# Kernel tuning notes

Measured on AMD Instinct MI355X. Metric: run time of the kernel, lower is better.

Reference implementation:

```python
import jax, jax.numpy as jnp
import numpy as np

P = 2          # feature power
K = 128        # top-k neighbors
ALPHA = 1.0
BETA = 1.0
EPS = 1e-12


def _smooth_rank_l2(v):
    # v: [B, r]. torch: relu(-(v[:,None,:] - v[:,:,None])).sum(-1)
    # element [b,i,j] of diff = v[b,j] - v[b,i]; relu(-diff) = relu(v[b,i]-v[b,j])
    return jnp.sum(jax.nn.relu(v[:, :, None] - v[:, None, :]), axis=-1)  # [B, r]


def setup_inputs() -> dict:
    key = jax.random.key(0)
    k1, k2, k3 = jax.random.split(key, 3)
    B, d, N0 = 256, 2048, 7936
    return {
        "f_s": jax.random.normal(k1, (B, d), dtype=jnp.float32),
        "f_t": jax.random.normal(k2, (B, d), dtype=jnp.float32),
        "gallery": jax.random.normal(k3, (N0, d), dtype=jnp.float32),
    }


def reference(f_s, f_t, gallery):
    # pool='all': x.pow(p).view(B, -1)
    fs = f_s ** P                      # [B, d]
    ft = f_t ** P                      # [B, d]
    # statistics=True, layer 0: teacher_features = concat(existing, f_t)
    gal = jnp.concatenate([gallery, ft], axis=0)   # [N, d]

    d2 = (jnp.sum(ft * ft, axis=-1, keepdims=True)
          + jnp.sum(gal * gal, axis=-1)[None, :]
          - 2.0 * ft @ gal.T)                       # [B, N]
    tt_dist = jnp.sqrt(jnp.clip(d2, EPS, None))

    # k smallest distances (torch.sort ascending + slice [:k])
    neg_top, top_k_index = jax.lax.top_k(-tt_dist, K)
    t_value = -neg_top                               # [B, K], ascending

    # per-row re-gather of gallery and student-to-gallery distances
    gal_k = gal[top_k_index]                         # [B, K, d]
    s_d2 = (jnp.sum(fs * fs, axis=-1)[:, None]
            + jnp.sum(gal_k * gal_k, axis=-1)
            - 2.0 * jnp.einsum('bd,bkd->bk', fs, gal_k))
    s_value = jnp.sqrt(jnp.clip(s_d2, EPS, None))    # [B, K]

    main_loss = ALPHA * jnp.mean(jnp.abs(s_value[:, 0] - t_value[:, 0]))

    r = K - 1
    t_rank = _smooth_rank_l2(t_value[:, 1:])         # [B, r]
    s_rank = _smooth_rank_l2(s_value[:, 1:])         # [B, r]
    extra_loss = BETA * jnp.mean(jnp.linalg.norm(t_rank - s_rank, axis=1)) / r

    return main_loss + extra_loss
```

## Files before the change

### kernel.cpp

```cpp
#include <hip/hip_runtime.h>
#include <hip/hip_bf16.h>

#define BDIM 256
#define DDIM 2048
#define NGAL 7936
#define NTOT 8192
#define TOPK 128
#define EPSC 1e-12f

typedef __attribute__((ext_vector_type(8))) short bf16x8;
typedef __attribute__((ext_vector_type(4))) float f32x4;
typedef unsigned long long u64;

__device__ __forceinline__ short bfr(float x) {
  unsigned u = __float_as_uint(x);
  unsigned r = (u + 0x7FFFu + ((u >> 16) & 1u)) >> 16;
  return (short)r;
}

__global__ __launch_bounds__(256) void k_prep(
    const float* __restrict__ f_t, const float* __restrict__ f_s,
    short* __restrict__ Abf, short* __restrict__ Bbf,
    float* __restrict__ normA, float* __restrict__ galnorm) {
  int b = blockIdx.x, t = threadIdx.x;
  const float4* t4 = (const float4*)(f_t + (size_t)b * DDIM);
  const float4* s4 = (const float4*)(f_s + (size_t)b * DDIM);
  float st = 0.f, ss = 0.f;
  for (int i = t; i < DDIM / 4; i += 256) {
    float4 v = t4[i];
    float4 q = make_float4(v.x * v.x, v.y * v.y, v.z * v.z, v.w * v.w);
    short4 qb = make_short4(bfr(q.x), bfr(q.y), bfr(q.z), bfr(q.w));
    *(short4*)&Abf[(size_t)b * DDIM + i * 4] = qb;
    *(short4*)&Bbf[(size_t)(NGAL + b) * DDIM + i * 4] = qb;
    st += q.x * q.x + q.y * q.y + q.z * q.z + q.w * q.w;
    float4 u_ = s4[i];
    float4 r = make_float4(u_.x * u_.x, u_.y * u_.y, u_.z * u_.z, u_.w * u_.w);
    *(short4*)&Abf[(size_t)(BDIM + b) * DDIM + i * 4] =
        make_short4(bfr(r.x), bfr(r.y), bfr(r.z), bfr(r.w));
    ss += r.x * r.x + r.y * r.y + r.z * r.z + r.w * r.w;
  }
  for (int off = 32; off; off >>= 1) {
    st += __shfl_xor(st, off);
    ss += __shfl_xor(ss, off);
  }
  __shared__ float red[8];
  int lane = t & 63, wv = t >> 6;
  if (lane == 0) { red[wv] = st; red[4 + wv] = ss; }
  __syncthreads();
  if (t == 0) {
    float a = red[0] + red[1] + red[2] + red[3];
    float c = red[4] + red[5] + red[6] + red[7];
    normA[b] = a;
    galnorm[NGAL + b] = a;
    normA[BDIM + b] = c;
  }
}

__global__ __launch_bounds__(256) void k_galn(
    const float* __restrict__ gallery, short* __restrict__ Bbf,
    float* __restrict__ galnorm) {
  int row = blockIdx.x * 4 + (threadIdx.x >> 6);
  int lane = threadIdx.x & 63;
  const float4* g4 = (const float4*)(gallery + (size_t)row * DDIM);
  float s = 0.f;
  for (int i = lane; i < DDIM / 4; i += 64) {
    float4 v = g4[i];
    *(short4*)&Bbf[(size_t)row * DDIM + i * 4] =
        make_short4(bfr(v.x), bfr(v.y), bfr(v.z), bfr(v.w));
    s += v.x * v.x + v.y * v.y + v.z * v.z + v.w * v.w;
  }
  for (int off = 32; off; off >>= 1) s += __shfl_xor(s, off);
  if (lane == 0) galnorm[row] = s;
}

__global__ __launch_bounds__(256) void k_gemm(
    const short* __restrict__ Abf, const short* __restrict__ Bbf,
    const float* __restrict__ normA, const float* __restrict__ galnorm,
    float* __restrict__ d2) {
  __shared__ short As[2][128 * 64];
  __shared__ short Bs[2][128 * 64];
  int t = threadIdx.x;
  int n0 = blockIdx.x * 128, m0 = blockIdx.y * 128;
  int lane = t & 63, wid = t >> 6;
  int wm = wid >> 1, wn = wid & 1;

  const short* Ag = Abf + (size_t)m0 * DDIM;
  const short* Bg = Bbf + (size_t)n0 * DDIM;

  int j = t & 7, rb_ = t >> 3;
  size_t gofs = (size_t)rb_ * DDIM + j * 8;
  int lofs = rb_ * 64 + ((j * 8) ^ ((rb_ & 7) << 3));

  int fr = lane & 15, fk = (lane >> 4) * 8;
  int axor = (fr & 7) << 3;

  f32x4 acc[4][4] = {};
  bf16x8 ra[4], rbv[4];

#pragma unroll
  for (int q = 0; q < 4; ++q) {
    ra[q] = *(const bf16x8*)(Ag + gofs + (size_t)q * 32 * DDIM);
    rbv[q] = *(const bf16x8*)(Bg + gofs + (size_t)q * 32 * DDIM);
  }
#pragma unroll
  for (int q = 0; q < 4; ++q) {
    *(bf16x8*)&As[0][lofs + q * 2048] = ra[q];
    *(bf16x8*)&Bs[0][lofs + q * 2048] = rbv[q];
  }
  int cur = 0;
  for (int kt = 0; kt < DDIM; kt += 64) {
    __syncthreads();
    bool more = (kt + 64) < DDIM;
    if (more) {
#pragma unroll
      for (int q = 0; q < 4; ++q) {
        ra[q] = *(const bf16x8*)(Ag + gofs + (size_t)q * 32 * DDIM + kt + 64);
        rbv[q] = *(const bf16x8*)(Bg + gofs + (size_t)q * 32 * DDIM + kt + 64);
      }
    }
#pragma unroll
    for (int ks = 0; ks < 2; ++ks) {
      int ko = (ks * 32 + fk) ^ axor;
      bf16x8 av[4], bv[4];
#pragma unroll
      for (int mi = 0; mi < 4; ++mi)
        av[mi] = *(const bf16x8*)&As[cur][(wm * 64 + mi * 16 + fr) * 64 + ko];
#pragma unroll
      for (int ni = 0; ni < 4; ++ni)
        bv[ni] = *(const bf16x8*)&Bs[cur][(wn * 64 + ni * 16 + fr) * 64 + ko];
#pragma unroll
      for (int mi = 0; mi < 4; ++mi)
#pragma unroll
        for (int ni = 0; ni < 4; ++ni)
          acc[mi][ni] = __builtin_amdgcn_mfma_f32_16x16x32_bf16(
              av[mi], bv[ni], acc[mi][ni], 0, 0, 0);
    }
    __syncthreads();
    if (more) {
      cur ^= 1;
#pragma unroll
      for (int q = 0; q < 4; ++q) {
        *(bf16x8*)&As[cur][lofs + q * 2048] = ra[q];
        *(bf16x8*)&Bs[cur][lofs + q * 2048] = rbv[q];
      }
    }
  }
  int rrow = (lane >> 4) * 4;
#pragma unroll
  for (int mi = 0; mi < 4; ++mi) {
#pragma unroll
    for (int r = 0; r < 4; ++r) {
      int m = m0 + wm * 64 + mi * 16 + rrow + r;
      float nm = normA[m];
#pragma unroll
      for (int ni = 0; ni < 4; ++ni) {
        int n = n0 + wn * 64 + ni * 16 + fr;
        float v = nm + galnorm[n] - 2.0f * acc[mi][ni][r];
        v = fmaxf(v, EPSC);
        if (m < BDIM && n == NGAL + m) v = EPSC;
        d2[(size_t)m * NTOT + n] = v;
      }
    }
  }
}

__global__ __launch_bounds__(256) void k_topk(
    const float* __restrict__ d2, float* __restrict__ t_value,
    int* __restrict__ topidx) {
  __shared__ float rowv[NTOT];
  __shared__ unsigned hist[4][256];
  __shared__ unsigned scan[256];
  __shared__ u64 cand[256];
  __shared__ unsigned s_pref, s_kneed, s_cnt;
  int b = blockIdx.x, t = threadIdx.x, w = t >> 6;
  const float4* row4 = (const float4*)(d2 + (size_t)b * NTOT);
  float4* rv4 = (float4*)rowv;
  for (int i = t; i < NTOT / 4; i += 256) rv4[i] = row4[i];
  if (t == 0) { s_pref = 0; s_kneed = TOPK; s_cnt = 0; }
  __syncthreads();
#pragma unroll 1
  for (int pass = 0; pass < 4; ++pass) {
    int shift = 24 - 8 * pass;
    unsigned prefmask = pass ? (0xFFFFFFFFu << (shift + 8)) : 0u;
    for (int i = t; i < 1024; i += 256) (&hist[0][0])[i] = 0;
    __syncthreads();
    unsigned pref = s_pref, kn = s_kneed;
    for (int i = t; i < NTOT; i += 256) {
      unsigned u = __float_as_uint(rowv[i]);
      if ((u & prefmask) == pref)
        atomicAdd(&hist[w][(u >> shift) & 255], 1u);
    }
    __syncthreads();
    unsigned h = hist[0][t] + hist[1][t] + hist[2][t] + hist[3][t];
    scan[t] = h;
    __syncthreads();
    for (int off = 1; off < 256; off <<= 1) {
      unsigned v_ = (t >= off) ? scan[t - off] : 0u;
      __syncthreads();
      scan[t] += v_;
      __syncthreads();
    }
    unsigned incl = scan[t], excl = incl - h;
    if (excl < kn && kn <= incl) {
      s_pref = pref | ((unsigned)t << shift);
      s_kneed = kn - excl;
    }
    __syncthreads();
  }
  unsigned ustar = s_pref;
  for (int i = t; i < NTOT; i += 256) {
    unsigned u = __float_as_uint(rowv[i]);
    if (u <= ustar) {
      unsigned p = atomicAdd(&s_cnt, 1u);
      if (p < 256) cand[p] = ((u64)u << 32) | (unsigned)i;
    }
  }
  __syncthreads();
  unsigned cnt = s_cnt;
  if (cnt > 256) cnt = 256;
  if (t >= (int)cnt) cand[t] = ~0ULL;
  __syncthreads();
  for (int len = 2; len <= 256; len <<= 1) {
    for (int inc = len >> 1; inc; inc >>= 1) {
      if (t < 128) {
        int low = t & (inc - 1);
        int i0 = ((t - low) << 1) + low, i1 = i0 + inc;
        u64 a = cand[i0], c = cand[i1];
        bool asc = ((i0 & len) == 0);
        if ((a > c) == asc) { cand[i0] = c; cand[i1] = a; }
      }
      __syncthreads();
    }
  }
  if (t < TOPK) {
    u64 kk = cand[t];
    t_value[b * TOPK + t] = sqrtf(__uint_as_float((unsigned)(kk >> 32)));
    topidx[b * TOPK + t] = (int)(unsigned)kk;
  }
}

__global__ __launch_bounds__(128) void k_sg(
    const float* __restrict__ d2, const int* __restrict__ topidx,
    float* __restrict__ s_value) {
  int b = blockIdx.x, t = threadIdx.x;
  int idx = topidx[b * TOPK + t];
  s_value[b * TOPK + t] = sqrtf(d2[(size_t)(BDIM + b) * NTOT + idx]);
}

__global__ __launch_bounds__(128) void k_loss(
    const float* __restrict__ t_value, const float* __restrict__ s_value,
    float* __restrict__ out) {
  __shared__ float tv[127], sv[127], red[2];
  int b = blockIdx.x, t = threadIdx.x;
  if (t < 127) {
    tv[t] = t_value[b * TOPK + 1 + t];
    sv[t] = s_value[b * TOPK + 1 + t];
  }
  __syncthreads();
  float val = 0.f;
  if (t < 127) {
    float ti = tv[t], si = sv[t], tr = 0.f, sr = 0.f;
    for (int j = 0; j < 127; ++j) {
      tr += fmaxf(ti - tv[j], 0.f);
      sr += fmaxf(si - sv[j], 0.f);
    }
    float d = tr - sr;
    val = d * d;
  }
  for (int off = 32; off; off >>= 1) val += __shfl_xor(val, off);
  int lane = t & 63, w = t >> 6;
  if (lane == 0) red[w] = val;
  __syncthreads();
  if (t == 0) {
    float sum = red[0] + red[1];
    float contrib =
        (1.0f / 256.0f) * fabsf(s_value[b * TOPK] - t_value[b * TOPK]) +
        (1.0f / (127.0f * 256.0f)) * sqrtf(sum);
    atomicAdd(out, contrib);
  }
}

extern "C" void kernel_launch(void* const* d_in, const int* in_sizes, int n_in,
                              void* d_out, int out_size, void* d_ws,
                              size_t ws_size, hipStream_t stream) {
  const float* f_s = (const float*)d_in[0];
  const float* f_t = (const float*)d_in[1];
  const float* gallery = (const float*)d_in[2];
  float* out = (float*)d_out;

  float* d2 = (float*)d_ws;
  short* Abf = (short*)(d2 + (size_t)512 * NTOT);
  short* Bbf = Abf + (size_t)512 * DDIM;
  float* normA = (float*)(Bbf + (size_t)NTOT * DDIM);
  float* galnorm = normA + 512;
  float* t_value = galnorm + NTOT;
  float* s_value = t_value + BDIM * TOPK;
  int* topidx = (int*)(s_value + BDIM * TOPK);

  hipMemsetAsync(d_out, 0, sizeof(float), stream);

  k_prep<<<BDIM, 256, 0, stream>>>(f_t, f_s, Abf, Bbf, normA, galnorm);
  k_galn<<<NGAL / 4, 256, 0, stream>>>(gallery, Bbf, galnorm);
  k_gemm<<<dim3(NTOT / 128, 512 / 128), 256, 0, stream>>>(Abf, Bbf, normA,
                                                          galnorm, d2);
  k_topk<<<BDIM, 256, 0, stream>>>(d2, t_value, topidx);
  k_sg<<<BDIM, 128, 0, stream>>>(d2, topidx, s_value);
  k_loss<<<BDIM, 128, 0, stream>>>(t_value, s_value, out);
}
```

Measured before the change: 182.2 us.

## Use direct-to-LDS loads in GEMM, radix-select top-k without sort, fuse gather

The GEMM now uses 64x128 tiles and stages tiles with global_load_lds straight into shared memory, with the swizzle applied on the global side. This removes the register round trip and doubles the block count. Top-k uses a 45-bit key (value plus index) with three 12-bit and one 9-bit radix passes and a shuffle-based scan, and writes selected elements unsorted. That drops the bitonic sort and folds the student gather into it. The loss kernel now finds the minimum element itself and excludes it from the rank sums. The risk is nondeterministic output order and reliance on the direct-LDS load semantics.

```diff
diff --git a/kernel.cpp b/kernel.cpp
--- a/kernel.cpp
+++ b/kernel.cpp
@@ -77,80 +77,76 @@
     const short* __restrict__ Abf, const short* __restrict__ Bbf,
     const float* __restrict__ normA, const float* __restrict__ galnorm,
     float* __restrict__ d2) {
-  __shared__ short As[2][128 * 64];
-  __shared__ short Bs[2][128 * 64];
+  __shared__ short S[2][12288];
   int t = threadIdx.x;
-  int n0 = blockIdx.x * 128, m0 = blockIdx.y * 128;
+  int n0 = blockIdx.x * 128, m0 = blockIdx.y * 64;
   int lane = t & 63, wid = t >> 6;
   int wm = wid >> 1, wn = wid & 1;
 
-  const short* Ag = Abf + (size_t)m0 * DDIM;
-  const short* Bg = Bbf + (size_t)n0 * DDIM;
-
-  int j = t & 7, rb_ = t >> 3;
-  size_t gofs = (size_t)rb_ * DDIM + j * 8;
-  int lofs = rb_ * 64 + ((j * 8) ^ ((rb_ & 7) << 3));
+  const short* gb[6];
+  int lof[6];
+#pragma unroll
+  for (int q = 0; q < 6; ++q) {
+    int c = t + q * 256;
+    int r, j;
+    const short* base;
+    if (c < 512) {
+      r = c >> 3; j = c & 7;
+      base = Abf + (size_t)(m0 + r) * DDIM;
+    } else {
+      int cb = c - 512;
+      r = cb >> 3; j = cb & 7;
+      base = Bbf + (size_t)(n0 + r) * DDIM;
+    }
+    gb[q] = base + ((j * 8) ^ ((r & 7) << 3));
+    lof[q] = c * 8;
+  }
 
   int fr = lane & 15, fk = (lane >> 4) * 8;
   int axor = (fr & 7) << 3;
-
-  f32x4 acc[4][4] = {};
-  bf16x8 ra[4], rbv[4];
-
-#pragma unroll
-  for (int q = 0; q < 4; ++q) {
-    ra[q] = *(const bf16x8*)(Ag + gofs + (size_t)q * 32 * DDIM);
-    rbv[q] = *(const bf16x8*)(Bg + gofs + (size_t)q * 32 * DDIM);
-  }
-#pragma unroll
-  for (int q = 0; q < 4; ++q) {
-    *(bf16x8*)&As[0][lofs + q * 2048] = ra[q];
-    *(bf16x8*)&Bs[0][lofs + q * 2048] = rbv[q];
-  }
+  f32x4 acc[2][4] = {};
+
+#define STAGE(buf, kt)                                                       \
+  {                                                                          \
+    _Pragma("unroll") for (int q = 0; q < 6; ++q)                            \
+        __builtin_amdgcn_global_load_lds(                                    \
+            (const __attribute__((address_space(1))) void*)(gb[q] + (kt)),   \
+            (__attribute__((address_space(3))) void*)(&S[buf][lof[q]]), 16,  \
+            0, 0);                                                           \
+  }
+
+  STAGE(0, 0);
+  __syncthreads();
   int cur = 0;
-  for (int kt = 0; kt < DDIM; kt += 64) {
-    __syncthreads();
-    bool more = (kt + 64) < DDIM;
-    if (more) {
-#pragma unroll
-      for (int q = 0; q < 4; ++q) {
-        ra[q] = *(const bf16x8*)(Ag + gofs + (size_t)q * 32 * DDIM + kt + 64);
-        rbv[q] = *(const bf16x8*)(Bg + gofs + (size_t)q * 32 * DDIM + kt + 64);
-      }
-    }
+  for (int it = 0; it < DDIM / 64; ++it) {
+    if (it + 1 < DDIM / 64) STAGE(cur ^ 1, (it + 1) * 64);
 #pragma unroll
     for (int ks = 0; ks < 2; ++ks) {
       int ko = (ks * 32 + fk) ^ axor;
-      bf16x8 av[4], bv[4];
-#pragma unroll
-      for (int mi = 0; mi < 4; ++mi)
-        av[mi] = *(const bf16x8*)&As[cur][(wm * 64 + mi * 16 + fr) * 64 + ko];
+      bf16x8 av[2], bv[4];
+#pragma unroll
+      for (int mi = 0; mi < 2; ++mi)
+        av[mi] = *(const bf16x8*)&S[cur][(wm * 32 + mi * 16 + fr) * 64 + ko];
 #pragma unroll
       for (int ni = 0; ni < 4; ++ni)
-        bv[ni] = *(const bf16x8*)&Bs[cur][(wn * 64 + ni * 16 + fr) * 64 + ko];
-#pragma unroll
-      for (int mi = 0; mi < 4; ++mi)
+        bv[ni] =
+            *(const bf16x8*)&S[cur][4096 + (wn * 64 + ni * 16 + fr) * 64 + ko];
+#pragma unroll
+      for (int mi = 0; mi < 2; ++mi)
 #pragma unroll
         for (int ni = 0; ni < 4; ++ni)
           acc[mi][ni] = __builtin_amdgcn_mfma_f32_16x16x32_bf16(
               av[mi], bv[ni], acc[mi][ni], 0, 0, 0);
     }
     __syncthreads();
-    if (more) {
-      cur ^= 1;
-#pragma unroll
-      for (int q = 0; q < 4; ++q) {
-        *(bf16x8*)&As[cur][lofs + q * 2048] = ra[q];
-        *(bf16x8*)&Bs[cur][lofs + q * 2048] = rbv[q];
-      }
-    }
+    cur ^= 1;
   }
   int rrow = (lane >> 4) * 4;
 #pragma unroll
-  for (int mi = 0; mi < 4; ++mi) {
+  for (int mi = 0; mi < 2; ++mi) {
 #pragma unroll
     for (int r = 0; r < 4; ++r) {
-      int m = m0 + wm * 64 + mi * 16 + rrow + r;
+      int m = m0 + wm * 32 + mi * 16 + rrow + r;
       float nm = normA[m];
 #pragma unroll
       for (int ni = 0; ni < 4; ++ni) {
@@ -162,120 +158,126 @@
       }
     }
   }
+#undef STAGE
 }
 
 __global__ __launch_bounds__(256) void k_topk(
     const float* __restrict__ d2, float* __restrict__ t_value,
-    int* __restrict__ topidx) {
-  __shared__ float rowv[NTOT];
-  __shared__ unsigned hist[4][256];
-  __shared__ unsigned scan[256];
-  __shared__ u64 cand[256];
-  __shared__ unsigned s_pref, s_kneed, s_cnt;
-  int b = blockIdx.x, t = threadIdx.x, w = t >> 6;
-  const float4* row4 = (const float4*)(d2 + (size_t)b * NTOT);
-  float4* rv4 = (float4*)rowv;
-  for (int i = t; i < NTOT / 4; i += 256) rv4[i] = row4[i];
+    float* __restrict__ s_value, int* __restrict__ topidx) {
+  __shared__ unsigned rowu[NTOT];
+  __shared__ unsigned hist[2][4096];
+  __shared__ unsigned wsum[4];
+  __shared__ u64 s_pref;
+  __shared__ unsigned s_kneed, s_cnt;
+  int b = blockIdx.x, t = threadIdx.x;
+  int lane = t & 63, w = t >> 6;
+  const uint4* r4 = (const uint4*)(d2 + (size_t)b * NTOT);
+  uint4* rv4 = (uint4*)rowu;
+  for (int i = t; i < NTOT / 4; i += 256) rv4[i] = r4[i];
   if (t == 0) { s_pref = 0; s_kneed = TOPK; s_cnt = 0; }
-  __syncthreads();
+
+  const int shs[4] = {33, 21, 9, 0};
+  const int bts[4] = {12, 12, 12, 9};
 #pragma unroll 1
-  for (int pass = 0; pass < 4; ++pass) {
-    int shift = 24 - 8 * pass;
-    unsigned prefmask = pass ? (0xFFFFFFFFu << (shift + 8)) : 0u;
-    for (int i = t; i < 1024; i += 256) (&hist[0][0])[i] = 0;
-    __syncthreads();
-    unsigned pref = s_pref, kn = s_kneed;
-    for (int i = t; i < NTOT; i += 256) {
-      unsigned u = __float_as_uint(rowv[i]);
-      if ((u & prefmask) == pref)
-        atomicAdd(&hist[w][(u >> shift) & 255], 1u);
-    }
-    __syncthreads();
-    unsigned h = hist[0][t] + hist[1][t] + hist[2][t] + hist[3][t];
-    scan[t] = h;
-    __syncthreads();
-    for (int off = 1; off < 256; off <<= 1) {
-      unsigned v_ = (t >= off) ? scan[t - off] : 0u;
-      __syncthreads();
-      scan[t] += v_;
-      __syncthreads();
-    }
-    unsigned incl = scan[t], excl = incl - h;
+  for (int p = 0; p < 4; ++p) {
+    int sh = shs[p], bits = bts[p];
+    unsigned nb = 1u << bits;
+    for (int i = t; i < 8192; i += 256) hist[0][i] = 0;
+    __syncthreads();
+    u64 pref = s_pref;
+    unsigned kn = s_kneed;
+    int sh_hi = sh + bits;
+#pragma unroll 1
+    for (int s = 0; s < NTOT / 256; ++s) {
+      int i = t + s * 256;
+      u64 key = ((u64)rowu[i] << 13) | (unsigned)i;
+      if ((key >> sh_hi) == pref)
+        atomicAdd(&hist[w & 1][(unsigned)(key >> sh) & (nb - 1)], 1u);
+    }
+    __syncthreads();
+    unsigned nbper = nb >> 8;
+    unsigned base = t * nbper, ls = 0;
+    for (unsigned j = 0; j < nbper; ++j)
+      ls += hist[0][base + j] + hist[1][base + j];
+    unsigned incl = ls;
+    for (int off = 1; off < 64; off <<= 1) {
+      unsigned x = __shfl_up(incl, off);
+      if (lane >= off) incl += x;
+    }
+    if (lane == 63) wsum[w] = incl;
+    __syncthreads();
+    unsigned woff = 0;
+    for (int ww = 0; ww < w; ++ww) woff += wsum[ww];
+    incl += woff;
+    unsigned excl = incl - ls;
     if (excl < kn && kn <= incl) {
-      s_pref = pref | ((unsigned)t << shift);
-      s_kneed = kn - excl;
-    }
-    __syncthreads();
-  }
-  unsigned ustar = s_pref;
-  for (int i = t; i < NTOT; i += 256) {
-    unsigned u = __float_as_uint(rowv[i]);
-    if (u <= ustar) {
-      unsigned p = atomicAdd(&s_cnt, 1u);
-      if (p < 256) cand[p] = ((u64)u << 32) | (unsigned)i;
-    }
-  }
-  __syncthreads();
-  unsigned cnt = s_cnt;
-  if (cnt > 256) cnt = 256;
-  if (t >= (int)cnt) cand[t] = ~0ULL;
-  __syncthreads();
-  for (int len = 2; len <= 256; len <<= 1) {
-    for (int inc = len >> 1; inc; inc >>= 1) {
-      if (t < 128) {
-        int low = t & (inc - 1);
-        int i0 = ((t - low) << 1) + low, i1 = i0 + inc;
-        u64 a = cand[i0], c = cand[i1];
-        bool asc = ((i0 & len) == 0);
-        if ((a > c) == asc) { cand[i0] = c; cand[i1] = a; }
+      unsigned re = excl, binj = 0;
+      for (unsigned j = 0; j < nbper; ++j) {
+        unsigned h = hist[0][base + j] + hist[1][base + j];
+        if (kn <= re + h) { binj = base + j; break; }
+        re += h;
       }
-      __syncthreads();
-    }
-  }
-  if (t < TOPK) {
-    u64 kk = cand[t];
-    t_value[b * TOPK + t] = sqrtf(__uint_as_float((unsigned)(kk >> 32)));
-    topidx[b * TOPK + t] = (int)(unsigned)kk;
-  }
-}
-
-__global__ __launch_bounds__(128) void k_sg(
-    const float* __restrict__ d2, const int* __restrict__ topidx,
-    float* __restrict__ s_value) {
-  int b = blockIdx.x, t = threadIdx.x;
-  int idx = topidx[b * TOPK + t];
-  s_value[b * TOPK + t] = sqrtf(d2[(size_t)(BDIM + b) * NTOT + idx]);
+      s_pref = (pref << bits) | binj;
+      s_kneed = kn - re;
+    }
+    __syncthreads();
+  }
+  u64 kstar = s_pref;
+  const float* srow = d2 + (size_t)(BDIM + b) * NTOT;
+#pragma unroll 1
+  for (int s = 0; s < NTOT / 256; ++s) {
+    int i = t + s * 256;
+    unsigned u = rowu[i];
+    u64 key = ((u64)u << 13) | (unsigned)i;
+    if (key <= kstar) {
+      unsigned pos = atomicAdd(&s_cnt, 1u);
+      t_value[b * TOPK + pos] = sqrtf(__uint_as_float(u));
+      s_value[b * TOPK + pos] = sqrtf(srow[i]);
+      topidx[b * TOPK + pos] = i;
+    }
+  }
 }
 
 __global__ __launch_bounds__(128) void k_loss(
     const float* __restrict__ t_value, const float* __restrict__ s_value,
-    float* __restrict__ out) {
-  __shared__ float tv[127], sv[127], red[2];
+    const int* __restrict__ topidx, float* __restrict__ out) {
   int b = blockIdx.x, t = threadIdx.x;
-  if (t < 127) {
-    tv[t] = t_value[b * TOPK + 1 + t];
-    sv[t] = s_value[b * TOPK + 1 + t];
-  }
-  __syncthreads();
-  float val = 0.f;
-  if (t < 127) {
-    float ti = tv[t], si = sv[t], tr = 0.f, sr = 0.f;
-    for (int j = 0; j < 127; ++j) {
-      tr += fmaxf(ti - tv[j], 0.f);
-      sr += fmaxf(si - sv[j], 0.f);
-    }
-    float d = tr - sr;
-    val = d * d;
-  }
-  for (int off = 32; off; off >>= 1) val += __shfl_xor(val, off);
+  float tv = t_value[b * TOPK + t], sv = s_value[b * TOPK + t];
+  int idx = topidx[b * TOPK + t];
+  u64 key = ((u64)__float_as_uint(tv) << 13) | (unsigned)idx;
+  u64 m_ = key;
+  for (int off = 1; off < 64; off <<= 1) {
+    u64 o = __shfl_xor(m_, off);
+    if (o < m_) m_ = o;
+  }
+  __shared__ u64 wmin[2];
+  __shared__ float tvs[TOPK], svs[TOPK], red[2], tm_s, sm_s;
   int lane = t & 63, w = t >> 6;
+  if (lane == 0) wmin[w] = m_;
+  tvs[t] = tv;
+  svs[t] = sv;
+  __syncthreads();
+  u64 kmin = wmin[0] < wmin[1] ? wmin[0] : wmin[1];
+  bool ismin = (key == kmin);
+  if (ismin) { tm_s = tv; sm_s = sv; }
+  __syncthreads();
+  float tmv = tm_s, smv = sm_s;
+  float tr = 0.f, sr = 0.f;
+  for (int j = 0; j < TOPK; ++j) {
+    tr += fmaxf(tv - tvs[j], 0.f);
+    sr += fmaxf(sv - svs[j], 0.f);
+  }
+  tr -= fmaxf(tv - tmv, 0.f);
+  sr -= fmaxf(sv - smv, 0.f);
+  float d = tr - sr;
+  float val = ismin ? 0.f : d * d;
+  for (int off = 1; off < 64; off <<= 1) val += __shfl_xor(val, off);
   if (lane == 0) red[w] = val;
   __syncthreads();
   if (t == 0) {
     float sum = red[0] + red[1];
-    float contrib =
-        (1.0f / 256.0f) * fabsf(s_value[b * TOPK] - t_value[b * TOPK]) +
-        (1.0f / (127.0f * 256.0f)) * sqrtf(sum);
+    float contrib = (1.f / 256.f) * fabsf(smv - tmv) +
+                    (1.f / (127.f * 256.f)) * sqrtf(sum);
     atomicAdd(out, contrib);
   }
 }
@@ -301,9 +303,8 @@
 
   k_prep<<<BDIM, 256, 0, stream>>>(f_t, f_s, Abf, Bbf, normA, galnorm);
   k_galn<<<NGAL / 4, 256, 0, stream>>>(gallery, Bbf, galnorm);
-  k_gemm<<<dim3(NTOT / 128, 512 / 128), 256, 0, stream>>>(Abf, Bbf, normA,
-                                                          galnorm, d2);
-  k_topk<<<BDIM, 256, 0, stream>>>(d2, t_value, topidx);
-  k_sg<<<BDIM, 128, 0, stream>>>(d2, topidx, s_value);
-  k_loss<<<BDIM, 128, 0, stream>>>(t_value, s_value, out);
-}
+  k_gemm<<<dim3(NTOT / 128, 512 / 64), 256, 0, stream>>>(Abf, Bbf, normA,
+                                                         galnorm, d2);
+  k_topk<<<BDIM, 256, 0, stream>>>(d2, t_value, s_value, topidx);
+  k_loss<<<BDIM, 128, 0, stream>>>(t_value, s_value, topidx, out);
+}
```

Measured after the change: 174.9 us. 1.04x faster.
